# Kernel tuning notes

Hardware: AMD Instinct MI355X
Metric: run time of the kernel (lower is better)

## Reference

```python
import jax, jax.numpy as jnp
import numpy as np

ENCODER_DIM, HIDDEN_DIM, ATT_DIM = 2048, 1024, 1024
B, P = 128, 196  # batch, num_pixels


def setup_inputs() -> dict:
    key = jax.random.key(0)
    ks = jax.random.split(key, 8)
    s_e = 1.0 / np.sqrt(ENCODER_DIM)
    s_h = 1.0 / np.sqrt(HIDDEN_DIM)
    s_a = 1.0 / np.sqrt(ATT_DIM)
    return {
        "encoder_out": jax.random.normal(ks[0], (B, P, ENCODER_DIM), jnp.float32),
        "decoder_hidden": jax.random.normal(ks[1], (B, HIDDEN_DIM), jnp.float32),
        # nn.Linear params (weight is [out, in] in torch; store transposed for x @ W)
        "W_enc": jax.random.uniform(ks[2], (ENCODER_DIM, ATT_DIM), jnp.float32, -s_e, s_e),
        "b_enc": jax.random.uniform(ks[3], (ATT_DIM,), jnp.float32, -s_e, s_e),
        "W_dec": jax.random.uniform(ks[4], (HIDDEN_DIM, ATT_DIM), jnp.float32, -s_h, s_h),
        "b_dec": jax.random.uniform(ks[5], (ATT_DIM,), jnp.float32, -s_h, s_h),
        "W_full": jax.random.uniform(ks[6], (ATT_DIM,), jnp.float32, -s_a, s_a),
        "b_full": jax.random.uniform(ks[7], (), jnp.float32, -s_a, s_a),
    }


def reference(encoder_out, decoder_hidden, W_enc, b_enc, W_dec, b_dec, W_full, b_full):
    # att1: [B, P, A]; att2: [B, 1, A]
    att1 = jnp.einsum("bpe,ea->bpa", encoder_out, W_enc) + b_enc
    att2 = decoder_hidden @ W_dec + b_dec
    att = jax.nn.relu(att1 + att2[:, None, :])
    scores = jnp.einsum("bpa,a->bp", att, W_full) + b_full  # [B, P]
    alpha = jax.nn.softmax(scores, axis=1)
    context = jnp.einsum("bpe,bp->be", encoder_out, alpha)  # [B, E]
    return (context, alpha)
```

## Files before the change

kernel.cpp:

```cpp
#include <hip/hip_runtime.h>
#include <hip/hip_bf16.h>


#define B_   128
#define P_   196
#define E_   2048
#define H_   1024
#define A_   1024
#define M_   (B_ * P_)
#define NKSTEP (E_ / 64)

typedef __bf16 bf16x8 __attribute__((ext_vector_type(8)));
typedef float f32x4 __attribute__((ext_vector_type(4)));

__device__ __bf16 g_wt[(size_t)A_ * E_];

__device__ __forceinline__ bf16x8 cvt8r(const float4 a, const float4 b) {
    bf16x8 r;
    r[0] = (__bf16)a.x; r[1] = (__bf16)a.y; r[2] = (__bf16)a.z; r[3] = (__bf16)a.w;
    r[4] = (__bf16)b.x; r[5] = (__bf16)b.y; r[6] = (__bf16)b.z; r[7] = (__bf16)b.w;
    return r;
}

__device__ __forceinline__ void gl16(const void* g, void* l) {
    __builtin_amdgcn_global_load_lds(
        (const __attribute__((address_space(1))) unsigned int*)g,
        (__attribute__((address_space(3))) unsigned int*)l, 16, 0, 0);
}

__global__ __launch_bounds__(256) void k_wt(const float* __restrict__ w) {
    __shared__ __bf16 tile[64][72];
    const int t = threadIdx.x;
    const int a0 = blockIdx.x * 64, e0 = blockIdx.y * 64;
    const int er = t >> 2, c0 = (t & 3) * 16;
#pragma unroll
    for (int j = 0; j < 4; ++j) {
        const float4 v =
            *(const float4*)&w[(size_t)(e0 + er) * A_ + a0 + c0 + j * 4];
        tile[c0 + j * 4 + 0][er] = (__bf16)v.x;
        tile[c0 + j * 4 + 1][er] = (__bf16)v.y;
        tile[c0 + j * 4 + 2][er] = (__bf16)v.z;
        tile[c0 + j * 4 + 3][er] = (__bf16)v.w;
    }
    __syncthreads();
    const int ar = t >> 2, es0 = (t & 3) * 16;
    *(bf16x8*)&g_wt[(size_t)(a0 + ar) * E_ + e0 + es0] =
        *(const bf16x8*)&tile[ar][es0];
    *(bf16x8*)&g_wt[(size_t)(a0 + ar) * E_ + e0 + es0 + 8] =
        *(const bf16x8*)&tile[ar][es0 + 8];
}

__global__ __launch_bounds__(256) void k_att2(
    const float* __restrict__ dh, const float* __restrict__ wdec,
    const float* __restrict__ benc, const float* __restrict__ bdec,
    float* __restrict__ scores, float* __restrict__ att2p) {
    const int t = threadIdx.x;
    const int a0 = blockIdx.x * 128;
    const int b0 = blockIdx.y * 8;
    const int bid = blockIdx.y * 8 + blockIdx.x;
    const int gi = bid * 256 + t;
    if (gi < M_) scores[gi] = 0.f;
    __shared__ float hs[8][H_];
    __shared__ float red[256][8];
    for (int i = t; i < 8 * H_; i += 256)
        hs[i >> 10][i & 1023] = dh[(size_t)(b0 + (i >> 10)) * H_ + (i & 1023)];
    __syncthreads();
    const int a = a0 + (t & 127);
    const int h0 = (t >> 7) * 512;
    float acc[8] = {};
#pragma unroll 4
    for (int h = 0; h < 512; ++h) {
        const float w = wdec[(size_t)(h0 + h) * A_ + a];
#pragma unroll
        for (int j = 0; j < 8; ++j) acc[j] += hs[j][h0 + h] * w;
    }
#pragma unroll
    for (int j = 0; j < 8; ++j) red[t][j] = acc[j];
    __syncthreads();
    if (t < 128) {
        const float bb = benc[a0 + t] + bdec[a0 + t];
#pragma unroll
        for (int j = 0; j < 8; ++j)
            att2p[(size_t)(b0 + j) * A_ + a0 + t] =
                red[t][j] + red[t + 128][j] + bb;
    }
}

__global__ __launch_bounds__(256, 2) void k_gemm_scores(
    const float* __restrict__ Am,
    const float* __restrict__ att2p,
    const float* __restrict__ wfull,
    float* __restrict__ scores) {
    __shared__ __align__(16) __bf16 As[2][128 * 72];
    __shared__ __align__(16) __bf16 Bs[2][128 * 64];
    __shared__ float red[2][128];

    const int t = threadIdx.x;
    const int lane = t & 63;
    const int wave = t >> 6;
    const int wm = wave >> 1, wn = wave & 1;
    const int q = lane >> 4, r = lane & 15;
    const int orig = blockIdx.y * 8 + blockIdx.x;
    const int L = (orig & 7) * (M_ / 128) + (orig >> 3);
    const int bn = L & 7, bm = L >> 3;
    const int m0 = bm * 128, n0 = bn * 128;

    const int srow = t >> 3;
    const int sseg = t & 7;
    const float* aptr = Am + (size_t)(m0 + srow) * E_ + sseg * 8;
    const int bswz = (((t & 7) ^ ((t >> 3) & 7)) << 4);
    const char* wt0 =
        (const char*)g_wt + (size_t)(n0 + srow) * (E_ * 2) + bswz;
    char* bdst0 = (char*)&Bs[0][0] + wave * 1024;
    char* bdst1 = (char*)&Bs[1][0] + wave * 1024;

    f32x4 acc[4][4] = {};
    float4 areg[8];

#pragma unroll
    for (int i = 0; i < 4; ++i) {
        const float* p = aptr + (size_t)(i * 32) * E_;
        areg[2 * i]     = *(const float4*)p;
        areg[2 * i + 1] = *(const float4*)(p + 4);
    }
#pragma unroll
    for (int i = 0; i < 4; ++i)
        gl16(wt0 + (size_t)i * (32 * E_ * 2), bdst0 + i * 4096);
#pragma unroll
    for (int i = 0; i < 4; ++i)
        *(bf16x8*)&As[0][(srow + i * 32) * 72 + sseg * 8] =
            cvt8r(areg[2 * i], areg[2 * i + 1]);

    int cur = 0;
#pragma unroll 2
    for (int kt = 0; kt < NKSTEP; ++kt) {
        asm volatile("s_waitcnt vmcnt(0)" ::: "memory");
        asm volatile("s_waitcnt lgkmcnt(0)" ::: "memory");
        __builtin_amdgcn_s_barrier();

        const __bf16* AsC = &As[cur][0];
        __bf16* AsN = &As[cur ^ 1][0];
        const char* BsC = (const char*)&Bs[cur][0];
        char* bdstN = cur ? bdst0 : bdst1;
        const bool pf = (kt + 1 < NKSTEP);

        if (pf) {
            const float* pa = aptr + (size_t)(kt + 1) * 64;
#pragma unroll
            for (int i = 0; i < 4; ++i) {
                const float* p = pa + (size_t)(i * 32) * E_;
                areg[2 * i]     = *(const float4*)p;
                areg[2 * i + 1] = *(const float4*)(p + 4);
            }
#pragma unroll
            for (int i = 0; i < 4; ++i)
                gl16(wt0 + (size_t)i * (32 * E_ * 2) + (size_t)(kt + 1) * 128,
                     bdstN + i * 4096);
        }

#pragma unroll
        for (int ks = 0; ks < 2; ++ks) {
            bf16x8 af[4], bfv[4];
#pragma unroll
            for (int f = 0; f < 4; ++f)
                af[f] = *(const bf16x8*)&AsC[(wm * 64 + f * 16 + r) * 72 +
                                             ks * 32 + q * 8];
#pragma unroll
            for (int f = 0; f < 4; ++f) {
                const int nf = wn * 64 + f * 16 + r;
                bfv[f] = *(const bf16x8*)(BsC + nf * 128 +
                         ((ks * 64 + q * 16) ^ ((r & 7) << 4)));
            }
#pragma unroll
            for (int fm = 0; fm < 4; ++fm)
#pragma unroll
                for (int fn = 0; fn < 4; ++fn)
                    acc[fm][fn] = __builtin_amdgcn_mfma_f32_16x16x32_bf16(
                        af[fm], bfv[fn], acc[fm][fn], 0, 0, 0);
        }

        if (pf) {
#pragma unroll
            for (int i = 0; i < 4; ++i)
                *(bf16x8*)&AsN[(srow + i * 32) * 72 + sseg * 8] =
                    cvt8r(areg[2 * i], areg[2 * i + 1]);
        }
        cur ^= 1;
    }

    float psum[4][4];
    const float* wfb = wfull + n0 + wn * 64;
#pragma unroll
    for (int fm = 0; fm < 4; ++fm) {
#pragma unroll
        for (int i = 0; i < 4; ++i) {
            const int row_g = m0 + wm * 64 + fm * 16 + q * 4 + i;
            const unsigned bidx = (unsigned)row_g / 196u;
            const float* a2 = att2p + (size_t)bidx * A_ + n0 + wn * 64;
            float s = 0.f;
#pragma unroll
            for (int fn = 0; fn < 4; ++fn) {
                const int cl = fn * 16 + r;
                float v = acc[fm][fn][i] + a2[cl];
                v = fmaxf(v, 0.f);
                s += v * wfb[cl];
            }
            psum[fm][i] = s;
        }
    }
#pragma unroll
    for (int fm = 0; fm < 4; ++fm)
#pragma unroll
        for (int i = 0; i < 4; ++i) {
            float v = psum[fm][i];
            v += __shfl_xor(v, 1);
            v += __shfl_xor(v, 2);
            v += __shfl_xor(v, 4);
            v += __shfl_xor(v, 8);
            if (r == 0) red[wn][wm * 64 + fm * 16 + q * 4 + i] = v;
        }
    __syncthreads();
    if (t < 128) atomicAdd(&scores[m0 + t], red[0][t] + red[1][t]);
}

__global__ __launch_bounds__(256) void k_softmax(
    const float* __restrict__ scores, float* __restrict__ out) {
    const int b = blockIdx.x;
    const int t = threadIdx.x;
    __shared__ float sm[256];
    const bool act = t < P_;
    const float val = act ? scores[b * P_ + t] : 0.f;
    sm[t] = act ? val : -1e30f;
    __syncthreads();
    for (int off = 128; off > 0; off >>= 1) {
        if (t < off) sm[t] = fmaxf(sm[t], sm[t + off]);
        __syncthreads();
    }
    const float mx = sm[0];
    __syncthreads();
    const float e = act ? __expf(val - mx) : 0.f;
    sm[t] = e;
    __syncthreads();
    for (int off = 128; off > 0; off >>= 1) {
        if (t < off) sm[t] = sm[t] + sm[t + off];
        __syncthreads();
    }
    const float inv = 1.0f / sm[0];
    if (act) out[(size_t)B_ * E_ + b * P_ + t] = e * inv;
}

__global__ __launch_bounds__(256) void k_context(
    const float* __restrict__ enc, float* __restrict__ out) {
    const int b = blockIdx.y;
    const int e0 = blockIdx.x * 1024 + threadIdx.x * 4;
    __shared__ float al[P_];
    if (threadIdx.x < P_)
        al[threadIdx.x] = out[(size_t)B_ * E_ + b * P_ + threadIdx.x];
    __syncthreads();
    float ax = 0.f, ay = 0.f, az = 0.f, aw = 0.f;
    const float* base = enc + (size_t)b * P_ * E_ + e0;
#pragma unroll 14
    for (int p = 0; p < P_; ++p) {
        const float4 v = *(const float4*)(base + (size_t)p * E_);
        const float ap = al[p];
        ax += ap * v.x; ay += ap * v.y; az += ap * v.z; aw += ap * v.w;
    }
    float4 sv; sv.x = ax; sv.y = ay; sv.z = az; sv.w = aw;
    *(float4*)(out + (size_t)b * E_ + e0) = sv;
}

extern "C" void kernel_launch(void* const* d_in, const int* in_sizes, int n_in,
                              void* d_out, int out_size, void* d_ws,
                              size_t ws_size, hipStream_t stream) {
    const float* enc   = (const float*)d_in[0];
    const float* dh    = (const float*)d_in[1];
    const float* wenc  = (const float*)d_in[2];
    const float* benc  = (const float*)d_in[3];
    const float* wdec  = (const float*)d_in[4];
    const float* bdec  = (const float*)d_in[5];
    const float* wfull = (const float*)d_in[6];
    float* out = (float*)d_out;

    float* att2p  = out;
    float* scores = (float*)((char*)d_out + 524288);

    k_wt<<<dim3(A_ / 64, E_ / 64), 256, 0, stream>>>(wenc);
    k_att2<<<dim3(8, 16), 256, 0, stream>>>(dh, wdec, benc, bdec, scores,
                                            att2p);
    k_gemm_scores<<<dim3(8, M_ / 128), 256, 0, stream>>>(enc, att2p, wfull,
                                                         scores);
    k_softmax<<<B_, 256, 0, stream>>>(scores, out);
    k_context<<<dim3(2, B_), 256, 0, stream>>>(enc, out);
}
```

Measured before the change: 553.7 us.

## Pre-convert encoder_out to bf16 and load GEMM A tiles via direct-to-LDS

A separate kernel now converts the whole fp32 encoder_out to a bf16 global buffer before the score GEMM. The GEMM then loads its A tiles with global_load_lds into a swizzled LDS layout, the same way it already loads B, so the register staging and per-tile conversion drop out of the inner loop. The cost is an extra pass that reads about 205 MB of fp32 and writes about 103 MB of bf16, plus a large global scratch array. The GEMM itself reads half as many A bytes, and its main loop becomes simpler and better overlapped.

```diff
diff --git a/kernel.cpp b/kernel.cpp
--- a/kernel.cpp
+++ b/kernel.cpp
@@ -14,6 +14,7 @@
 typedef float f32x4 __attribute__((ext_vector_type(4)));
 
 __device__ __bf16 g_wt[(size_t)A_ * E_];
+__device__ __bf16 g_enc[(size_t)M_ * E_];
 
 __device__ __forceinline__ bf16x8 cvt8r(const float4 a, const float4 b) {
     bf16x8 r;
@@ -26,6 +27,17 @@
     __builtin_amdgcn_global_load_lds(
         (const __attribute__((address_space(1))) unsigned int*)g,
         (__attribute__((address_space(3))) unsigned int*)l, 16, 0, 0);
+}
+
+__global__ __launch_bounds__(256) void k_cvt(const float* __restrict__ enc) {
+    const size_t n = (size_t)M_ * E_;
+    const size_t stride = (size_t)gridDim.x * 256 * 8;
+    for (size_t i = ((size_t)blockIdx.x * 256 + threadIdx.x) * 8; i < n;
+         i += stride) {
+        const float4 a = *(const float4*)(enc + i);
+        const float4 b = *(const float4*)(enc + i + 4);
+        *(bf16x8*)&g_enc[i] = cvt8r(a, b);
+    }
 }
 
 __global__ __launch_bounds__(256) void k_wt(const float* __restrict__ w) {
@@ -87,11 +99,10 @@
 }
 
 __global__ __launch_bounds__(256, 2) void k_gemm_scores(
-    const float* __restrict__ Am,
     const float* __restrict__ att2p,
     const float* __restrict__ wfull,
     float* __restrict__ scores) {
-    __shared__ __align__(16) __bf16 As[2][128 * 72];
+    __shared__ __align__(16) __bf16 As[2][128 * 64];
     __shared__ __align__(16) __bf16 Bs[2][128 * 64];
     __shared__ float red[2][128];
 
@@ -105,71 +116,59 @@
     const int bn = L & 7, bm = L >> 3;
     const int m0 = bm * 128, n0 = bn * 128;
 
-    const int srow = t >> 3;
-    const int sseg = t & 7;
-    const float* aptr = Am + (size_t)(m0 + srow) * E_ + sseg * 8;
-    const int bswz = (((t & 7) ^ ((t >> 3) & 7)) << 4);
-    const char* wt0 =
-        (const char*)g_wt + (size_t)(n0 + srow) * (E_ * 2) + bswz;
-    char* bdst0 = (char*)&Bs[0][0] + wave * 1024;
-    char* bdst1 = (char*)&Bs[1][0] + wave * 1024;
+    const int rbase = wave * 8 + (lane >> 3);
+    const int cx = ((t & 7) ^ ((t >> 3) & 7)) * 16;
+    const char* pa = (const char*)g_enc + (size_t)(m0 + rbase) * 4096 + cx;
+    const char* pb = (const char*)g_wt  + (size_t)(n0 + rbase) * 4096 + cx;
+    char* ad0 = (char*)&As[0][0] + wave * 1024;
+    char* ad1 = (char*)&As[1][0] + wave * 1024;
+    char* bd0 = (char*)&Bs[0][0] + wave * 1024;
+    char* bd1 = (char*)&Bs[1][0] + wave * 1024;
 
     f32x4 acc[4][4] = {};
-    float4 areg[8];
-
-#pragma unroll
-    for (int i = 0; i < 4; ++i) {
-        const float* p = aptr + (size_t)(i * 32) * E_;
-        areg[2 * i]     = *(const float4*)p;
-        areg[2 * i + 1] = *(const float4*)(p + 4);
-    }
+
 #pragma unroll
     for (int i = 0; i < 4; ++i)
-        gl16(wt0 + (size_t)i * (32 * E_ * 2), bdst0 + i * 4096);
+        gl16(pa + (size_t)i * 131072, ad0 + i * 4096);
 #pragma unroll
     for (int i = 0; i < 4; ++i)
-        *(bf16x8*)&As[0][(srow + i * 32) * 72 + sseg * 8] =
-            cvt8r(areg[2 * i], areg[2 * i + 1]);
+        gl16(pb + (size_t)i * 131072, bd0 + i * 4096);
 
     int cur = 0;
-#pragma unroll 2
     for (int kt = 0; kt < NKSTEP; ++kt) {
         asm volatile("s_waitcnt vmcnt(0)" ::: "memory");
         asm volatile("s_waitcnt lgkmcnt(0)" ::: "memory");
         __builtin_amdgcn_s_barrier();
 
-        const __bf16* AsC = &As[cur][0];
-        __bf16* AsN = &As[cur ^ 1][0];
+        const char* AsC = (const char*)&As[cur][0];
         const char* BsC = (const char*)&Bs[cur][0];
-        char* bdstN = cur ? bdst0 : bdst1;
-        const bool pf = (kt + 1 < NKSTEP);
-
-        if (pf) {
-            const float* pa = aptr + (size_t)(kt + 1) * 64;
-#pragma unroll
-            for (int i = 0; i < 4; ++i) {
-                const float* p = pa + (size_t)(i * 32) * E_;
-                areg[2 * i]     = *(const float4*)p;
-                areg[2 * i + 1] = *(const float4*)(p + 4);
-            }
+
+        if (kt + 1 < NKSTEP) {
+            char* ad = cur ? ad0 : ad1;
+            char* bd = cur ? bd0 : bd1;
+            const size_t ko = (size_t)(kt + 1) * 128;
 #pragma unroll
             for (int i = 0; i < 4; ++i)
-                gl16(wt0 + (size_t)i * (32 * E_ * 2) + (size_t)(kt + 1) * 128,
-                     bdstN + i * 4096);
+                gl16(pa + (size_t)i * 131072 + ko, ad + i * 4096);
+#pragma unroll
+            for (int i = 0; i < 4; ++i)
+                gl16(pb + (size_t)i * 131072 + ko, bd + i * 4096);
         }
 
 #pragma unroll
         for (int ks = 0; ks < 2; ++ks) {
             bf16x8 af[4], bfv[4];
 #pragma unroll
-            for (int f = 0; f < 4; ++f)
-                af[f] = *(const bf16x8*)&AsC[(wm * 64 + f * 16 + r) * 72 +
-                                             ks * 32 + q * 8];
+            for (int f = 0; f < 4; ++f) {
+                const int mf = wm * 64 + f * 16 + r;
+                af[f] = *(const bf16x8*)(AsC + mf * 128 +
+                        ((ks * 64 + q * 16) ^ ((r & 7) << 4)));
+            }
 #pragma unroll
             for (int f = 0; f < 4; ++f) {
                 const int nf = wn * 64 + f * 16 + r;
                 bfv[f] = *(const bf16x8*)(BsC + nf * 128 +
-                         ((ks * 64 + q * 16) ^ ((r & 7) << 4)));
+                        ((ks * 64 + q * 16) ^ ((r & 7) << 4)));
             }
 #pragma unroll
             for (int fm = 0; fm < 4; ++fm)
@@ -177,13 +176,6 @@
                 for (int fn = 0; fn < 4; ++fn)
                     acc[fm][fn] = __builtin_amdgcn_mfma_f32_16x16x32_bf16(
                         af[fm], bfv[fn], acc[fm][fn], 0, 0, 0);
-        }
-
-        if (pf) {
-#pragma unroll
-            for (int i = 0; i < 4; ++i)
-                *(bf16x8*)&AsN[(srow + i * 32) * 72 + sseg * 8] =
-                    cvt8r(areg[2 * i], areg[2 * i + 1]);
         }
         cur ^= 1;
     }
@@ -284,10 +276,11 @@
     float* att2p  = out;
     float* scores = (float*)((char*)d_out + 524288);
 
+    k_cvt<<<2048, 256, 0, stream>>>(enc);
     k_wt<<<dim3(A_ / 64, E_ / 64), 256, 0, stream>>>(wenc);
     k_att2<<<dim3(8, 16), 256, 0, stream>>>(dh, wdec, benc, bdec, scores,
                                             att2p);
-    k_gemm_scores<<<dim3(8, M_ / 128), 256, 0, stream>>>(enc, att2p, wfull,
+    k_gemm_scores<<<dim3(8, M_ / 128), 256, 0, stream>>>(att2p, wfull,
                                                          scores);
     k_softmax<<<B_, 256, 0, stream>>>(scores, out);
     k_context<<<dim3(2, B_), 256, 0, stream>>>(enc, out);
```

Result: slower. 595.4 us (+7.5%).
